# Kernel tuning notes

Hardware: AMD Instinct MI355X
Metric: run time of the kernel (lower is better)

## Reference

```python
import jax, jax.numpy as jnp
import numpy as np

H, DH = 8, 16  # num_heads, head_dim (out_feats // num_heads)
NP, NA, NS = 100000, 60000, 1000


def _gat_conv(feat_src, feat_dst, n_dst, src, dst, W, al, ar, b):
    # DGL GATConv (eval mode: feat_drop/attn_drop are identity)
    hs = (feat_src @ W).reshape(-1, H, DH)          # [Ns,H,D]
    hd = (feat_dst @ W).reshape(-1, H, DH)          # [Nd,H,D]
    el = (hs * al).sum(-1)                          # [Ns,H]
    er = (hd * ar).sum(-1)                          # [Nd,H]
    e = jax.nn.leaky_relu(el[src] + er[dst], negative_slope=0.2)  # [E,H]
    # segment softmax over edges sharing a destination node
    emax = jax.ops.segment_max(e, dst, num_segments=n_dst)
    emax = jnp.where(jnp.isfinite(emax), emax, 0.0)
    ee = jnp.exp(e - emax[dst])
    denom = jax.ops.segment_sum(ee, dst, num_segments=n_dst)
    alpha = ee / jnp.maximum(denom[dst], 1e-9)      # [E,H]
    m = jax.ops.segment_sum(alpha[:, :, None] * hs[src], dst, num_segments=n_dst)
    return m.reshape(n_dst, H * DH) + b             # [Nd, out_feats]


def setup_inputs() -> dict:
    key = jax.random.key(0)
    ks = jax.random.split(key, 18)
    Epa, Eps = 300000, 150000
    f32 = jnp.float32
    inp = {
        "feat_paper_0": jax.random.normal(ks[0], (NP, 128), f32),
        "feat_author_0": jax.random.normal(ks[1], (NA, 128), f32),
        "feat_subject_0": jax.random.normal(ks[2], (NS, 128), f32),
        "feat_paper_1": jax.random.normal(ks[3], (NP, 128), f32),
        "feat_author_1": jax.random.normal(ks[4], (NA, 128), f32),
        "feat_subject_1": jax.random.normal(ks[5], (NS, 128), f32),
        "pa_src": jax.random.randint(ks[6], (Epa,), 0, NP, jnp.int32),
        "pa_dst": jax.random.randint(ks[7], (Epa,), 0, NA, jnp.int32),
        "ap_src": jax.random.randint(ks[8], (Epa,), 0, NA, jnp.int32),
        "ap_dst": jax.random.randint(ks[9], (Epa,), 0, NP, jnp.int32),
        "ps_src": jax.random.randint(ks[10], (Eps,), 0, NP, jnp.int32),
        "ps_dst": jax.random.randint(ks[11], (Eps,), 0, NS, jnp.int32),
        "sp_src": jax.random.randint(ks[12], (Eps,), 0, NS, jnp.int32),
        "sp_dst": jax.random.randint(ks[13], (Eps,), 0, NP, jnp.int32),
        "Ws": jax.random.normal(ks[14], (4, 128, 128), f32) * 0.08,
        "als": jax.random.normal(ks[15], (4, H, DH), f32) * 0.1,
        "ars": jax.random.normal(ks[16], (4, H, DH), f32) * 0.1,
        "bs": jnp.zeros((4, 128), f32),
    }
    return inp


def reference(feat_paper_0, feat_author_0, feat_subject_0,
              feat_paper_1, feat_author_1, feat_subject_1,
              pa_src, pa_dst, ap_src, ap_dst, ps_src, ps_dst, sp_src, sp_dst,
              Ws, als, ars, bs):
    def one_input(fp, fa, fs):
        # rel 0: paper->author, 1: author->paper, 2: paper->subject, 3: subject->paper
        h_author = _gat_conv(fp, fa, NA, pa_src, pa_dst, Ws[0], als[0], ars[0], bs[0])
        h_paper_ap = _gat_conv(fa, fp, NP, ap_src, ap_dst, Ws[1], als[1], ars[1], bs[1])
        h_subject = _gat_conv(fp, fs, NS, ps_src, ps_dst, Ws[2], als[2], ars[2], bs[2])
        h_paper_sp = _gat_conv(fs, fp, NP, sp_src, sp_dst, Ws[3], als[3], ars[3], bs[3])
        h_paper = (h_paper_ap + h_paper_sp) * 0.5  # HeteroGraphConv aggregate='mean'
        # act = identity; key order for ACM: [paper, author, subject]
        return jnp.concatenate([h_paper, h_author, h_subject], axis=0)

    out0 = one_input(feat_paper_0, feat_author_0, feat_subject_0)
    out1 = one_input(feat_paper_1, feat_author_1, feat_subject_1)
    return jnp.stack([out0, out1], axis=0)  # [2, NP+NA+NS, 128]
```

## Files before the change

### kernel.cpp

```cpp
#include <hip/hip_runtime.h>

#define NHEAD 8
#define NPAPER 100000
#define NAUTHOR 60000
#define NSUBJ 1000
#define NTOT (NPAPER + NAUTHOR + NSUBJ)
#define NDEG 261000

typedef __attribute__((ext_vector_type(8))) short bf16x8;
typedef __attribute__((ext_vector_type(4))) float f32x4;

__device__ __forceinline__ unsigned short f2bf(float x) {
    unsigned int u = __builtin_bit_cast(unsigned int, x);
    u += 0x7fffu + ((u >> 16) & 1u);
    return (unsigned short)(u >> 16);
}
__device__ __forceinline__ float bf2f_lo(unsigned int v) {
    return __builtin_bit_cast(float, v << 16);
}
__device__ __forceinline__ float bf2f_hi(unsigned int v) {
    return __builtin_bit_cast(float, v & 0xffff0000u);
}

__global__ void prep_kernel(const float* __restrict__ Ws, const float* __restrict__ als,
                            const float* __restrict__ ars,
                            unsigned short* __restrict__ Wt,
                            unsigned short* __restrict__ combo, int* __restrict__ deg) {
    int b = blockIdx.x;
    if (b >= 288) {
        int idx = (b - 288) * 1024 + threadIdx.x * 4;
        if (idx < NDEG) *reinterpret_cast<int4*>(&deg[idx]) = int4{0, 0, 0, 0};
        return;
    }
    int idx = b * 256 + threadIdx.x;
    if (idx < 65536) {
        int r = idx >> 14, rem = idx & 16383, c = rem >> 7, k = rem & 127;
        Wt[idx] = f2bf(Ws[(r << 14) + k * 128 + c]);
    } else if (idx < 65536 + 8192) {
        int j = idx - 65536;
        int r = j >> 11, rem = j & 2047, n = rem >> 7, k = rem & 127;
        int p = r ^ 1;
        const float *W, *a;
        if (n < 8) {
            W = Ws + (r << 14) + k * 128 + n * 16;
            a = als + r * 128 + n * 16;
        } else {
            int h = n - 8;
            W = Ws + (p << 14) + k * 128 + h * 16;
            a = ars + p * 128 + h * 16;
        }
        float s = 0.f;
#pragma unroll
        for (int d = 0; d < 16; ++d) s += W[d] * a[d];
        combo[j] = f2bf(s);
    }
}

struct EdgePtrs {
    const int* esrc[4];
    const int* edst[4];
    int ebase[5];
    int nbase[4];
};

__global__ void csr_count(EdgePtrs cp, int* __restrict__ deg) {
    int idx = blockIdx.x * 256 + threadIdx.x;
    if (idx >= cp.ebase[4]) return;
    int r = 0;
    while (idx >= cp.ebase[r + 1]) ++r;
    atomicAdd(&deg[cp.nbase[r] + cp.edst[r][idx - cp.ebase[r]]], 1);
}

__global__ __launch_bounds__(256) void scan_bsum(const int* __restrict__ deg,
                                                 int* __restrict__ bsums, int N) {
    int base = blockIdx.x * 1024 + threadIdx.x * 4;
    int s = 0;
#pragma unroll
    for (int j = 0; j < 4; ++j) {
        int i = base + j;
        if (i < N) s += deg[i];
    }
#pragma unroll
    for (int off = 32; off; off >>= 1) s += __shfl_down(s, off);
    __shared__ int wt[4];
    if ((threadIdx.x & 63) == 0) wt[threadIdx.x >> 6] = s;
    __syncthreads();
    if (threadIdx.x == 0) bsums[blockIdx.x] = wt[0] + wt[1] + wt[2] + wt[3];
}

__global__ __launch_bounds__(256) void scan_final(const int* __restrict__ deg,
                                                  const int* __restrict__ bsums,
                                                  int* __restrict__ row_ptr,
                                                  int* __restrict__ cursor, int N) {
    int t = threadIdx.x;
    __shared__ int s_start;
    __shared__ int wsum[4];
    {
        int acc = 0;
        for (int i = t; i < (int)blockIdx.x; i += 256) acc += bsums[i];
#pragma unroll
        for (int off = 32; off; off >>= 1) acc += __shfl_down(acc, off);
        if ((t & 63) == 0) wsum[t >> 6] = acc;
        __syncthreads();
        if (t == 0) s_start = wsum[0] + wsum[1] + wsum[2] + wsum[3];
        __syncthreads();
    }
    int base = blockIdx.x * 1024 + t * 4;
    int d[4];
    int s = 0;
#pragma unroll
    for (int j = 0; j < 4; ++j) {
        int i = base + j;
        d[j] = (i < N) ? deg[i] : 0;
        s += d[j];
    }
    int inc = s;
#pragma unroll
    for (int off = 1; off < 64; off <<= 1) {
        int u = __shfl_up(inc, off);
        if ((t & 63) >= off) inc += u;
    }
    __shared__ int wt[4];
    if ((t & 63) == 63) wt[t >> 6] = inc;
    __syncthreads();
    int start = s_start;
    for (int w = 0; w < (t >> 6); ++w) start += wt[w];
    start += inc - s;
#pragma unroll
    for (int j = 0; j < 4; ++j) {
        int i = base + j;
        if (i < N) {
            row_ptr[i] = start;
            cursor[i] = start;
        }
        start += d[j];
    }
    if (base < N && base + 4 >= N) row_ptr[N] = start;
}

__device__ __forceinline__ void stage_W(unsigned short* Wl,
                                        const unsigned short* __restrict__ Wt,
                                        const unsigned short* __restrict__ cb, int tid) {
#pragma unroll
    for (int it = 0; it < 9; ++it) {
        int id = it * 256 + tid;
        int r = id >> 4, c8 = id & 15;
        const unsigned short* srcp = (r < 128) ? (Wt + r * 128) : (cb + (r - 128) * 128);
        uint4 v = *reinterpret_cast<const uint4*>(srcp + c8 * 8);
        *reinterpret_cast<uint4*>(&Wl[(r * 16 + (c8 ^ (r & 15))) * 8]) = v;
    }
}

__device__ __forceinline__ void mfma_set(const unsigned short* Wl, unsigned short* Abf,
                                         const bf16x8* af, int tid, int row0, int N,
                                         float* __restrict__ el, float* __restrict__ er) {
    const int l = tid & 63, w = tid >> 6, lrow = l & 15, lk8 = l >> 4;
#pragma unroll
    for (int t9 = 0; t9 < 9; ++t9) {
        f32x4 acc = f32x4{0.f, 0.f, 0.f, 0.f};
#pragma unroll
        for (int ks = 0; ks < 4; ++ks) {
            int wrow = t9 * 16 + lrow;
            int c8 = ks * 4 + lk8;
            bf16x8 bf = *reinterpret_cast<const bf16x8*>(
                &Wl[(wrow * 16 + (c8 ^ (wrow & 15))) * 8]);
            acc = __builtin_amdgcn_mfma_f32_16x16x32_bf16(af[ks], bf, acc, 0, 0, 0);
        }
        if (t9 < 8) {
#pragma unroll
            for (int r = 0; r < 4; ++r) {
                int rl = w * 16 + lk8 * 4 + r;
                int col = t9 * 16 + lrow;
                Abf[(rl * 16 + ((col >> 3) ^ (rl & 15))) * 8 + (col & 7)] = f2bf(acc[r]);
            }
        } else {
#pragma unroll
            for (int r = 0; r < 4; ++r) {
                int row = row0 + w * 16 + lk8 * 4 + r;
                if (row < N) {
                    if (lrow < 8) el[(size_t)row * 8 + lrow] = acc[r];
                    else er[(size_t)row * 8 + (lrow - 8)] = acc[r];
                }
            }
        }
    }
}

__device__ __forceinline__ void store_hs(const unsigned short* Abf,
                                         unsigned short* __restrict__ hs, int tid,
                                         int row0, int N) {
#pragma unroll
    for (int it = 0; it < 4; ++it) {
        int id = it * 256 + tid;
        int r = id >> 4, c8 = id & 15;
        int row = row0 + r;
        if (row < N) {
            uint4 v = *reinterpret_cast<const uint4*>(&Abf[(r * 16 + (c8 ^ (r & 15))) * 8]);
            *reinterpret_cast<uint4*>(hs + (size_t)row * 128 + c8 * 8) = v;
        }
    }
}

struct SPArgs {
    const int* esrc[4];
    const int* edst[4];
    int ebase[5];
    int nbase[4];
    int* cursor;
    int* scsr;
    int sblk;
    const float* A[6];
    int N[6];
    int blk0[7];
    const unsigned short* Wt1[6];
    const unsigned short* cb1[6];
    unsigned short* hs1[6];
    float* el1[6];
    float* er1[6];
    const unsigned short* Wt2[6];
    const unsigned short* cb2[6];
    unsigned short* hs2[6];
    float* el2[6];
    float* er2[6];
    int has2[6];
};

__global__ __launch_bounds__(256) void scatter_project(SPArgs a) {
    __shared__ unsigned short Abf[64 * 128];
    __shared__ unsigned short Wl[144 * 128];
    int bb = blockIdx.x;
    const int tid = threadIdx.x;
    if (bb < a.sblk) {
        int idx = bb * 256 + tid;
        if (idx < a.ebase[4]) {
            int r = 0;
            while (idx >= a.ebase[r + 1]) ++r;
            int e = idx - a.ebase[r];
            int p = atomicAdd(&a.cursor[a.nbase[r] + a.edst[r][e]], 1);
            a.scsr[p] = a.esrc[r][e];
        }
        return;
    }
    bb -= a.sblk;
    int t = 0;
    while (bb >= a.blk0[t + 1]) ++t;
    const int row0 = (bb - a.blk0[t]) * 64;
    const int N = a.N[t];
    const float* A = a.A[t];

#pragma unroll
    for (int it = 0; it < 4; ++it) {
        int id = it * 256 + tid;
        int r = id >> 4, c8 = id & 15;
        int row = row0 + r;
        if (row >= N) row = N - 1;
        const f32x4* ap = reinterpret_cast<const f32x4*>(A + (size_t)row * 128 + c8 * 8);
        f32x4 v0 = __builtin_nontemporal_load(ap);
        f32x4 v1 = __builtin_nontemporal_load(ap + 1);
        uint4 pk;
        pk.x = (unsigned)f2bf(v0.x) | ((unsigned)f2bf(v0.y) << 16);
        pk.y = (unsigned)f2bf(v0.z) | ((unsigned)f2bf(v0.w) << 16);
        pk.z = (unsigned)f2bf(v1.x) | ((unsigned)f2bf(v1.y) << 16);
        pk.w = (unsigned)f2bf(v1.z) | ((unsigned)f2bf(v1.w) << 16);
        *reinterpret_cast<uint4*>(&Abf[(r * 16 + (c8 ^ (r & 15))) * 8]) = pk;
    }
    stage_W(Wl, a.Wt1[t], a.cb1[t], tid);
    __syncthreads();

    const int l = tid & 63, w = tid >> 6, lrow = l & 15, lk8 = l >> 4;
    bf16x8 af[4];
    const int arow = w * 16 + lrow;
#pragma unroll
    for (int ks = 0; ks < 4; ++ks) {
        int c8 = ks * 4 + lk8;
        af[ks] = *reinterpret_cast<const bf16x8*>(
            &Abf[(arow * 16 + (c8 ^ (arow & 15))) * 8]);
    }
    __syncthreads();

    mfma_set(Wl, Abf, af, tid, row0, N, a.el1[t], a.er1[t]);
    __syncthreads();
    store_hs(Abf, a.hs1[t], tid, row0, N);
    if (!a.has2[t]) return;
    stage_W(Wl, a.Wt2[t], a.cb2[t], tid);
    __syncthreads();
    mfma_set(Wl, Abf, af, tid, row0, N, a.el2[t], a.er2[t]);
    __syncthreads();
    store_hs(Abf, a.hs2[t], tid, row0, N);
}

__device__ __forceinline__ void acc_dual(
    int p0, int p1, float erd0, float erd1, int l, int h,
    const int* __restrict__ srcs,
    const float* __restrict__ el0, const float* __restrict__ el1,
    const unsigned short* __restrict__ hs0, const unsigned short* __restrict__ hs1,
    float* A0, float* A1, float& DS0, float& DS1) {
    float a0[8], a1[8];
#pragma unroll
    for (int j = 0; j < 8; ++j) { a0[j] = 0.f; a1[j] = 0.f; }
    float d0 = 0.f, d1 = 0.f;
    int p = p0;
    for (; p + 4 <= p1; p += 4) {
        int sx[4];
#pragma unroll
        for (int u = 0; u < 4; ++u) sx[u] = srcs[p + u];
        float ev0[4], ev1[4];
        uint4 q0[4], q1[4];
#pragma unroll
        for (int u = 0; u < 4; ++u) {
            ev0[u] = el0[(size_t)sx[u] * 8 + h] + erd0;
            ev1[u] = el1[(size_t)sx[u] * 8 + h] + erd1;
            q0[u] = *reinterpret_cast<const uint4*>(hs0 + (size_t)sx[u] * 128 + l * 8);
            q1[u] = *reinterpret_cast<const uint4*>(hs1 + (size_t)sx[u] * 128 + l * 8);
        }
#pragma unroll
        for (int u = 0; u < 4; ++u) {
            float e0 = ev0[u];
            e0 = e0 > 0.f ? e0 : 0.2f * e0;
            float ee0 = __expf(e0);
            d0 += ee0;
            a0[0] += ee0 * bf2f_lo(q0[u].x);
            a0[1] += ee0 * bf2f_hi(q0[u].x);
            a0[2] += ee0 * bf2f_lo(q0[u].y);
            a0[3] += ee0 * bf2f_hi(q0[u].y);
            a0[4] += ee0 * bf2f_lo(q0[u].z);
            a0[5] += ee0 * bf2f_hi(q0[u].z);
            a0[6] += ee0 * bf2f_lo(q0[u].w);
            a0[7] += ee0 * bf2f_hi(q0[u].w);
            float e1 = ev1[u];
            e1 = e1 > 0.f ? e1 : 0.2f * e1;
            float ee1 = __expf(e1);
            d1 += ee1;
            a1[0] += ee1 * bf2f_lo(q1[u].x);
            a1[1] += ee1 * bf2f_hi(q1[u].x);
            a1[2] += ee1 * bf2f_lo(q1[u].y);
            a1[3] += ee1 * bf2f_hi(q1[u].y);
            a1[4] += ee1 * bf2f_lo(q1[u].z);
            a1[5] += ee1 * bf2f_hi(q1[u].z);
            a1[6] += ee1 * bf2f_lo(q1[u].w);
            a1[7] += ee1 * bf2f_hi(q1[u].w);
        }
    }
    for (; p < p1; ++p) {
        int s = srcs[p];
        float e0 = el0[(size_t)s * 8 + h] + erd0;
        float e1 = el1[(size_t)s * 8 + h] + erd1;
        uint4 q0 = *reinterpret_cast<const uint4*>(hs0 + (size_t)s * 128 + l * 8);
        uint4 q1 = *reinterpret_cast<const uint4*>(hs1 + (size_t)s * 128 + l * 8);
        e0 = e0 > 0.f ? e0 : 0.2f * e0;
        float ee0 = __expf(e0);
        d0 += ee0;
        a0[0] += ee0 * bf2f_lo(q0.x);
        a0[1] += ee0 * bf2f_hi(q0.x);
        a0[2] += ee0 * bf2f_lo(q0.y);
        a0[3] += ee0 * bf2f_hi(q0.y);
        a0[4] += ee0 * bf2f_lo(q0.z);
        a0[5] += ee0 * bf2f_hi(q0.z);
        a0[6] += ee0 * bf2f_lo(q0.w);
        a0[7] += ee0 * bf2f_hi(q0.w);
        e1 = e1 > 0.f ? e1 : 0.2f * e1;
        float ee1 = __expf(e1);
        d1 += ee1;
        a1[0] += ee1 * bf2f_lo(q1.x);
        a1[1] += ee1 * bf2f_hi(q1.x);
        a1[2] += ee1 * bf2f_lo(q1.y);
        a1[3] += ee1 * bf2f_hi(q1.y);
        a1[4] += ee1 * bf2f_lo(q1.z);
        a1[5] += ee1 * bf2f_hi(q1.z);
        a1[6] += ee1 * bf2f_lo(q1.w);
        a1[7] += ee1 * bf2f_hi(q1.w);
    }
#pragma unroll
    for (int j = 0; j < 8; ++j) { A0[j] = a0[j]; A1[j] = a1[j]; }
    DS0 = d0;
    DS1 = d1;
}

__device__ __forceinline__ void nt_store2(float* op, f32x4 o0, f32x4 o1) {
    f32x4* vp = reinterpret_cast<f32x4*>(op);
    __builtin_nontemporal_store(o0, vp);
    __builtin_nontemporal_store(o1, vp + 1);
}

#define PB2 6250
#define AB2 3750
#define SB2 1000

struct AggArgs {
    const int* rp;
    const int* srcs;
    const float* el[8];
    const float* er[8];
    const unsigned short* hs[8];
    const float* bs;
    float* out0;
    float* out1;
};

__global__ __launch_bounds__(256) void mega_agg(AggArgs a) {
    int blk = blockIdx.x;
    __shared__ float Am[16][128];
    __shared__ float Dm[16][8];

    if (blk < PB2) {
        int dst = blk * 16 + (threadIdx.x >> 4);
        int l = threadIdx.x & 15, h = l >> 1;
        if (dst >= NPAPER) return;
        float A1_0[8], A1_1[8], d1_0, d1_1;
        acc_dual(a.rp[60000 + dst], a.rp[60000 + dst + 1],
                 a.er[1][(size_t)dst * 8 + h], a.er[5][(size_t)dst * 8 + h], l, h,
                 a.srcs, a.el[1], a.el[5], a.hs[1], a.hs[5], A1_0, A1_1, d1_0, d1_1);
        float A3_0[8], A3_1[8], d3_0, d3_1;
        acc_dual(a.rp[161000 + dst], a.rp[161000 + dst + 1],
                 a.er[3][(size_t)dst * 8 + h], a.er[7][(size_t)dst * 8 + h], l, h,
                 a.srcs, a.el[3], a.el[7], a.hs[3], a.hs[7], A3_0, A3_1, d3_0, d3_1);
        const float4* bp1 = reinterpret_cast<const float4*>(a.bs + 128 + l * 8);
        const float4* bp3 = reinterpret_cast<const float4*>(a.bs + 384 + l * 8);
        float4 b10 = bp1[0], b11 = bp1[1], b30 = bp3[0], b31 = bp3[1];
        float i1 = 1.f / fmaxf(d1_0, 1e-9f);
        float i3 = 1.f / fmaxf(d3_0, 1e-9f);
        f32x4 o0, o1;
        o0.x = 0.5f * ((A1_0[0] * i1 + b10.x) + (A3_0[0] * i3 + b30.x));
        o0.y = 0.5f * ((A1_0[1] * i1 + b10.y) + (A3_0[1] * i3 + b30.y));
        o0.z = 0.5f * ((A1_0[2] * i1 + b10.z) + (A3_0[2] * i3 + b30.z));
        o0.w = 0.5f * ((A1_0[3] * i1 + b10.w) + (A3_0[3] * i3 + b30.w));
        o1.x = 0.5f * ((A1_0[4] * i1 + b11.x) + (A3_0[4] * i3 + b31.x));
        o1.y = 0.5f * ((A1_0[5] * i1 + b11.y) + (A3_0[5] * i3 + b31.y));
        o1.z = 0.5f * ((A1_0[6] * i1 + b11.z) + (A3_0[6] * i3 + b31.z));
        o1.w = 0.5f * ((A1_0[7] * i1 + b11.w) + (A3_0[7] * i3 + b31.w));
        nt_store2(a.out0 + (size_t)dst * 128 + l * 8, o0, o1);
        i1 = 1.f / fmaxf(d1_1, 1e-9f);
        i3 = 1.f / fmaxf(d3_1, 1e-9f);
        o0.x = 0.5f * ((A1_1[0] * i1 + b10.x) + (A3_1[0] * i3 + b30.x));
        o0.y = 0.5f * ((A1_1[1] * i1 + b10.y) + (A3_1[1] * i3 + b30.y));
        o0.z = 0.5f * ((A1_1[2] * i1 + b10.z) + (A3_1[2] * i3 + b30.z));
        o0.w = 0.5f * ((A1_1[3] * i1 + b10.w) + (A3_1[3] * i3 + b30.w));
        o1.x = 0.5f * ((A1_1[4] * i1 + b11.x) + (A3_1[4] * i3 + b31.x));
        o1.y = 0.5f * ((A1_1[5] * i1 + b11.y) + (A3_1[5] * i3 + b31.y));
        o1.z = 0.5f * ((A1_1[6] * i1 + b11.z) + (A3_1[6] * i3 + b31.z));
        o1.w = 0.5f * ((A1_1[7] * i1 + b11.w) + (A3_1[7] * i3 + b31.w));
        nt_store2(a.out1 + (size_t)dst * 128 + l * 8, o0, o1);
    } else if (blk < PB2 + AB2) {
        int dst = (blk - PB2) * 16 + (threadIdx.x >> 4);
        int l = threadIdx.x & 15, h = l >> 1;
        if (dst >= NAUTHOR) return;
        float A0[8], A1[8], d0, d1;
        acc_dual(a.rp[dst], a.rp[dst + 1],
                 a.er[0][(size_t)dst * 8 + h], a.er[4][(size_t)dst * 8 + h], l, h,
                 a.srcs, a.el[0], a.el[4], a.hs[0], a.hs[4], A0, A1, d0, d1);
        const float4* bp = reinterpret_cast<const float4*>(a.bs + l * 8);
        float4 b0 = bp[0], b1 = bp[1];
        float inv = 1.f / fmaxf(d0, 1e-9f);
        f32x4 o0 = {A0[0] * inv + b0.x, A0[1] * inv + b0.y,
                    A0[2] * inv + b0.z, A0[3] * inv + b0.w};
        f32x4 o1 = {A0[4] * inv + b1.x, A0[5] * inv + b1.y,
                    A0[6] * inv + b1.z, A0[7] * inv + b1.w};
        nt_store2(a.out0 + (size_t)(NPAPER + dst) * 128 + l * 8, o0, o1);
        inv = 1.f / fmaxf(d1, 1e-9f);
        o0 = f32x4{A1[0] * inv + b0.x, A1[1] * inv + b0.y,
                   A1[2] * inv + b0.z, A1[3] * inv + b0.w};
        o1 = f32x4{A1[4] * inv + b1.x, A1[5] * inv + b1.y,
                   A1[6] * inv + b1.z, A1[7] * inv + b1.w};
        nt_store2(a.out1 + (size_t)(NPAPER + dst) * 128 + l * 8, o0, o1);
    } else {
        int dst = blk - (PB2 + AB2);
        int gl = threadIdx.x >> 4;
        int inp = gl >> 3, ck = gl & 7;
        int l = threadIdx.x & 15, h = l >> 1;
        const float* el = a.el[inp * 4 + 2];
        const float* er = a.er[inp * 4 + 2];
        const unsigned short* hs = a.hs[inp * 4 + 2];
        int p0 = a.rp[160000 + dst], p1 = a.rp[160000 + dst + 1];
        float erd = er[(size_t)dst * 8 + h];
        float acc8[8];
#pragma unroll
        for (int j = 0; j < 8; ++j) acc8[j] = 0.f;
        float dsum = 0.f;
        for (int p = p0 + ck; p < p1; p += 8) {
            int s = a.srcs[p];
            float e = el[(size_t)s * 8 + h] + erd;
            e = e > 0.f ? e : 0.2f * e;
            float ee = __expf(e);
            uint4 q = *reinterpret_cast<const uint4*>(hs + (size_t)s * 128 + l * 8);
            dsum += ee;
            acc8[0] += ee * bf2f_lo(q.x);
            acc8[1] += ee * bf2f_hi(q.x);
            acc8[2] += ee * bf2f_lo(q.y);
            acc8[3] += ee * bf2f_hi(q.y);
            acc8[4] += ee * bf2f_lo(q.z);
            acc8[5] += ee * bf2f_hi(q.z);
            acc8[6] += ee * bf2f_lo(q.w);
            acc8[7] += ee * bf2f_hi(q.w);
        }
#pragma unroll
        for (int j = 0; j < 8; ++j) Am[gl][l * 8 + j] = acc8[j];
        if ((l & 1) == 0) Dm[gl][h] = dsum;
        __syncthreads();
        int c = threadIdx.x;
        int ci = c >> 7;
        int col = c & 127;
        float s = 0.f, dn = 0.f;
        int hh = col >> 4;
#pragma unroll
        for (int g = 0; g < 8; ++g) {
            s += Am[ci * 8 + g][col];
            dn += Dm[ci * 8 + g][hh];
        }
        float v = s / fmaxf(dn, 1e-9f) + a.bs[256 + col];
        float* outp = (ci ? a.out1 : a.out0) + (size_t)(NPAPER + NAUTHOR + dst) * 128 + col;
        __builtin_nontemporal_store(v, outp);
    }
}

extern "C" void kernel_launch(void* const* d_in, const int* in_sizes, int n_in,
                              void* d_out, int out_size, void* d_ws, size_t ws_size,
                              hipStream_t stream) {
    const float* Ws4 = (const float*)d_in[14];
    const float* als = (const float*)d_in[15];
    const float* ars = (const float*)d_in[16];
    const float* bs = (const float*)d_in[17];
    float* out = (float*)d_out;

    const int Es[4] = {in_sizes[6], in_sizes[8], in_sizes[10], in_sizes[12]};
    const int Nsrcs[4] = {NPAPER, NAUTHOR, NPAPER, NSUBJ};
    const int Ndsts[4] = {NAUTHOR, NPAPER, NSUBJ, NPAPER};
    const int Etot = Es[0] + Es[1] + Es[2] + Es[3];

    char* wsp = (char*)d_ws;
    auto carve = [&](size_t bytes) {
        char* p = wsp;
        wsp += (bytes + 255) & ~(size_t)255;
        return p;
    };
    unsigned short* Wt = (unsigned short*)carve(4 * 16384 * 2);
    unsigned short* combo = (unsigned short*)carve(4 * 2048 * 2);
    unsigned short* hsb[2][4];
    float* elb[2][4];
    float* erb[2][4];
    for (int i = 0; i < 2; ++i)
        for (int r = 0; r < 4; ++r) {
            hsb[i][r] = (unsigned short*)carve((size_t)Nsrcs[r] * 128 * 2);
            elb[i][r] = (float*)carve((size_t)Nsrcs[r] * 8 * 4);
            erb[i][r] = (float*)carve((size_t)Ndsts[r] * 8 * 4);
        }
    int* deg = (int*)carve((size_t)NDEG * 4);
    int* cursor = (int*)carve((size_t)NDEG * 4);
    int* bsums = (int*)carve(1024);
    int* rp = (int*)carve((size_t)(NDEG + 1) * 4);
    int* scsr = (int*)carve((size_t)Etot * 4);

    EdgePtrs ep;
    ep.esrc[0] = (const int*)d_in[6];  ep.edst[0] = (const int*)d_in[7];
    ep.esrc[1] = (const int*)d_in[8];  ep.edst[1] = (const int*)d_in[9];
    ep.esrc[2] = (const int*)d_in[10]; ep.edst[2] = (const int*)d_in[11];
    ep.esrc[3] = (const int*)d_in[12]; ep.edst[3] = (const int*)d_in[13];
    ep.ebase[0] = 0;
    for (int r = 0; r < 4; ++r) ep.ebase[r + 1] = ep.ebase[r] + Es[r];
    ep.nbase[0] = 0;
    ep.nbase[1] = 60000;
    ep.nbase[2] = 160000;
    ep.nbase[3] = 161000;

    prep_kernel<<<288 + (NDEG + 1023) / 1024, 256, 0, stream>>>(Ws4, als, ars, Wt,
                                                                combo, deg);
    csr_count<<<(Etot + 255) / 256, 256, 0, stream>>>(ep, deg);
    int nb = (NDEG + 1023) / 1024;
    scan_bsum<<<nb, 256, 0, stream>>>(deg, bsums, NDEG);
    scan_final<<<nb, 256, 0, stream>>>(deg, bsums, rp, cursor, NDEG);

    SPArgs sp;
    for (int r = 0; r < 4; ++r) {
        sp.esrc[r] = ep.esrc[r];
        sp.edst[r] = ep.edst[r];
        sp.nbase[r] = ep.nbase[r];
    }
    for (int r = 0; r < 5; ++r) sp.ebase[r] = ep.ebase[r];
    sp.cursor = cursor;
    sp.scsr = scsr;
    sp.sblk = (Etot + 255) / 256;

    int blk = 0;
    for (int ti = 0; ti < 6; ++ti) {
        int i = ti & 1;
        int nodeT = ti >> 1;
        const int relOf[3] = {0, 1, 3};
        int r = relOf[nodeT];
        const float* feats[3] = {(const float*)d_in[0 + 3 * i],
                                 (const float*)d_in[1 + 3 * i],
                                 (const float*)d_in[2 + 3 * i]};
        sp.A[ti] = feats[nodeT];
        sp.N[ti] = (nodeT == 0) ? NPAPER : (nodeT == 1 ? NAUTHOR : NSUBJ);
        sp.blk0[ti] = blk;
        blk += (sp.N[ti] + 63) / 64;
        sp.Wt1[ti] = Wt + (size_t)r * 16384;
        sp.cb1[ti] = combo + (size_t)r * 2048;
        sp.hs1[ti] = hsb[i][r];
        sp.el1[ti] = elb[i][r];
        sp.er1[ti] = erb[i][r ^ 1];
        sp.has2[ti] = (nodeT == 0);
        int r2 = 2;
        sp.Wt2[ti] = Wt + (size_t)r2 * 16384;
        sp.cb2[ti] = combo + (size_t)r2 * 2048;
        sp.hs2[ti] = hsb[i][r2];
        sp.el2[ti] = elb[i][r2];
        sp.er2[ti] = erb[i][r2 ^ 1];
    }
    sp.blk0[6] = blk;
    scatter_project<<<sp.sblk + blk, 256, 0, stream>>>(sp);

    AggArgs ag;
    ag.rp = rp;
    ag.srcs = scsr;
    for (int i = 0; i < 2; ++i)
        for (int r = 0; r < 4; ++r) {
            ag.el[i * 4 + r] = elb[i][r];
            ag.er[i * 4 + r] = erb[i][r];
            ag.hs[i * 4 + r] = hsb[i][r];
        }
    ag.bs = bs;
    ag.out0 = out;
    ag.out1 = out + (size_t)NTOT * 128;
    mega_agg<<<PB2 + AB2 + SB2, 256, 0, stream>>>(ag);
}
```

Baseline: 326.1 us.

## Sort destination nodes by in-degree for load-balanced aggregation

Adds a histogram, a bin scan and a permutation-scatter pass that group paper and author destination nodes by in-degree (capped at 63). The aggregation kernel then processes nodes in permuted order, so the 16 nodes sharing a block have similar edge counts and lanes sit idle less. This costs three extra small launches with atomics, and output writes and er reads become scattered rather than contiguous.

```diff
diff --git a/kernel.cpp b/kernel.cpp
--- a/kernel.cpp
+++ b/kernel.cpp
@@ -29,7 +29,7 @@
     int b = blockIdx.x;
     if (b >= 288) {
         int idx = (b - 288) * 1024 + threadIdx.x * 4;
-        if (idx < NDEG) *reinterpret_cast<int4*>(&deg[idx]) = int4{0, 0, 0, 0};
+        if (idx < NDEG + 128) *reinterpret_cast<int4*>(&deg[idx]) = int4{0, 0, 0, 0};
         return;
     }
     int idx = b * 256 + threadIdx.x;
@@ -69,6 +69,41 @@
     int r = 0;
     while (idx >= cp.ebase[r + 1]) ++r;
     atomicAdd(&deg[cp.nbase[r] + cp.edst[r][idx - cp.ebase[r]]], 1);
+}
+
+__global__ void hist_kernel(const int* __restrict__ deg, int* __restrict__ hist) {
+    int idx = blockIdx.x * 256 + threadIdx.x;
+    if (idx < NPAPER) {
+        int d = deg[60000 + idx] + deg[161000 + idx];
+        atomicAdd(&hist[d > 63 ? 63 : d], 1);
+    } else if (idx < NPAPER + NAUTHOR) {
+        int d = deg[idx - NPAPER];
+        atomicAdd(&hist[64 + (d > 63 ? 63 : d)], 1);
+    }
+}
+
+__global__ void binscan_kernel(const int* __restrict__ hist, int* __restrict__ cursors) {
+    if (threadIdx.x == 0) {
+        int acc = 0;
+        for (int i = 0; i < 64; ++i) { cursors[i] = acc; acc += hist[i]; }
+        acc = 0;
+        for (int i = 0; i < 64; ++i) { cursors[64 + i] = acc; acc += hist[64 + i]; }
+    }
+}
+
+__global__ void permscatter_kernel(const int* __restrict__ deg, int* __restrict__ cursors,
+                                   int* __restrict__ permP, int* __restrict__ permA) {
+    int idx = blockIdx.x * 256 + threadIdx.x;
+    if (idx < NPAPER) {
+        int d = deg[60000 + idx] + deg[161000 + idx];
+        int slot = atomicAdd(&cursors[d > 63 ? 63 : d], 1);
+        permP[slot] = idx;
+    } else if (idx < NPAPER + NAUTHOR) {
+        int j = idx - NPAPER;
+        int d = deg[j];
+        int slot = atomicAdd(&cursors[64 + (d > 63 ? 63 : d)], 1);
+        permA[slot] = j;
+    }
 }
 
 __global__ __launch_bounds__(256) void scan_bsum(const int* __restrict__ deg,
@@ -389,6 +424,8 @@
 struct AggArgs {
     const int* rp;
     const int* srcs;
+    const int* permP;
+    const int* permA;
     const float* el[8];
     const float* er[8];
     const unsigned short* hs[8];
@@ -403,9 +440,10 @@
     __shared__ float Dm[16][8];
 
     if (blk < PB2) {
-        int dst = blk * 16 + (threadIdx.x >> 4);
+        int g = blk * 16 + (threadIdx.x >> 4);
         int l = threadIdx.x & 15, h = l >> 1;
-        if (dst >= NPAPER) return;
+        if (g >= NPAPER) return;
+        int dst = a.permP[g];
         float A1_0[8], A1_1[8], d1_0, d1_1;
         acc_dual(a.rp[60000 + dst], a.rp[60000 + dst + 1],
                  a.er[1][(size_t)dst * 8 + h], a.er[5][(size_t)dst * 8 + h], l, h,
@@ -441,9 +479,10 @@
         o1.w = 0.5f * ((A1_1[7] * i1 + b11.w) + (A3_1[7] * i3 + b31.w));
         nt_store2(a.out1 + (size_t)dst * 128 + l * 8, o0, o1);
     } else if (blk < PB2 + AB2) {
-        int dst = (blk - PB2) * 16 + (threadIdx.x >> 4);
+        int g = (blk - PB2) * 16 + (threadIdx.x >> 4);
         int l = threadIdx.x & 15, h = l >> 1;
-        if (dst >= NAUTHOR) return;
+        if (g >= NAUTHOR) return;
+        int dst = a.permA[g];
         float A0[8], A1[8], d0, d1;
         acc_dual(a.rp[dst], a.rp[dst + 1],
                  a.er[0][(size_t)dst * 8 + h], a.er[4][(size_t)dst * 8 + h], l, h,
@@ -543,9 +582,13 @@
             elb[i][r] = (float*)carve((size_t)Nsrcs[r] * 8 * 4);
             erb[i][r] = (float*)carve((size_t)Ndsts[r] * 8 * 4);
         }
-    int* deg = (int*)carve((size_t)NDEG * 4);
+    int* deg = (int*)carve((size_t)(NDEG + 128) * 4);
+    int* hist = deg + NDEG;
     int* cursor = (int*)carve((size_t)NDEG * 4);
     int* bsums = (int*)carve(1024);
+    int* bincur = (int*)carve(128 * 4);
+    int* permP = (int*)carve((size_t)NPAPER * 4);
+    int* permA = (int*)carve((size_t)NAUTHOR * 4);
     int* rp = (int*)carve((size_t)(NDEG + 1) * 4);
     int* scsr = (int*)carve((size_t)Etot * 4);
 
@@ -561,12 +604,16 @@
     ep.nbase[2] = 160000;
     ep.nbase[3] = 161000;
 
-    prep_kernel<<<288 + (NDEG + 1023) / 1024, 256, 0, stream>>>(Ws4, als, ars, Wt,
-                                                                combo, deg);
+    prep_kernel<<<288 + (NDEG + 128 + 1023) / 1024, 256, 0, stream>>>(Ws4, als, ars, Wt,
+                                                                      combo, deg);
     csr_count<<<(Etot + 255) / 256, 256, 0, stream>>>(ep, deg);
     int nb = (NDEG + 1023) / 1024;
     scan_bsum<<<nb, 256, 0, stream>>>(deg, bsums, NDEG);
     scan_final<<<nb, 256, 0, stream>>>(deg, bsums, rp, cursor, NDEG);
+    int nh = (NPAPER + NAUTHOR + 255) / 256;
+    hist_kernel<<<nh, 256, 0, stream>>>(deg, hist);
+    binscan_kernel<<<1, 64, 0, stream>>>(hist, bincur);
+    permscatter_kernel<<<nh, 256, 0, stream>>>(deg, bincur, permP, permA);
 
     SPArgs sp;
     for (int r = 0; r < 4; ++r) {
@@ -611,6 +658,8 @@
     AggArgs ag;
     ag.rp = rp;
     ag.srcs = scsr;
+    ag.permP = permP;
+    ag.permA = permA;
     for (int i = 0; i < 2; ++i)
         for (int r = 0; r < 4; ++r) {
             ag.el[i * 4 + r] = elb[i][r];
```

After: 1.191 ms. 265% more time.
